# Performance work log

Measured on AMD Instinct MI355X. Metric: run time of the kernel, lower is better.

The kernel has to match this reference:

```python
import jax, jax.numpy as jnp
import numpy as np


def setup_inputs() -> dict:
    key = jax.random.key(0)
    k1, k2 = jax.random.split(key)
    x = jax.random.normal(k1, (8, 2500, 100), dtype=jnp.float32)          # [B, L, E]
    label_feature = jax.random.normal(k2, (8922, 100), dtype=jnp.float32)  # [N, E]
    return {"x": x, "label_feature": label_feature}


def reference(x, label_feature):
    # scores: [B, N, L] = label_feature @ x^T (broadcast query over batch), unscaled
    scores = jnp.einsum("ne,ble->bnl", label_feature, x)
    alpha = jax.nn.softmax(scores, axis=2)  # softmax over sequence length
    # m: [B, N, E] = alpha @ x
    m = jnp.einsum("bnl,ble->bne", alpha, x)
    return m
```

## Files before the change

### kernel.cpp

```cpp
#include <hip/hip_runtime.h>
#include <math.h>
#include <stdint.h>

typedef __attribute__((ext_vector_type(8))) _Float16 half8;
typedef __attribute__((ext_vector_type(4))) _Float16 half4;
typedef __attribute__((ext_vector_type(4))) float f32x4;

constexpr int Bb = 8, Ll = 2500, Ee = 100, Nn = 8922;
constexpr int LP = 2560, EP = 128;
constexpr int NP = 9024;
constexpr int VE = 112;
constexpr int LT = 64;
constexpr int NTILES = LP / LT;
constexpr int NTB = 192;
constexpr int NH = 3;

constexpr size_t SZ_LF = (size_t)NP * EP * 2;
constexpr size_t SZ_XW = (size_t)Bb * LP * EP * 2;
constexpr size_t SZ_XT = (size_t)Bb * VE * LP * 2;
constexpr size_t OFF_XW = SZ_LF;
constexpr size_t OFF_XT = OFF_XW + SZ_XW;
constexpr size_t WS_NEED = OFF_XT + SZ_XT;

__device__ __forceinline__ void gload16(const void* g, void* l) {
    __builtin_amdgcn_global_load_lds(
        (const __attribute__((address_space(1))) uint32_t*)g,
        (__attribute__((address_space(3))) uint32_t*)l, 16, 0, 0);
}

__global__ __launch_bounds__(256)
void prep_all(const float* __restrict__ x, const float* __restrict__ lf,
              uint32_t* __restrict__ dlf, uint32_t* __restrict__ dxw,
              uint16_t* __restrict__ dxt) {
    if (blockIdx.y == Bb) {
        for (int idx = blockIdx.x * 256 + threadIdx.x; idx < NP * 64; idx += 40 * 256) {
            int n = idx >> 6, ep = idx & 63;
            int e0 = 2 * ep, e1 = e0 + 1;
            float f0 = (n < Nn && e0 < Ee) ? lf[(size_t)n * Ee + e0] : 0.f;
            float f1 = (n < Nn && e1 < Ee) ? lf[(size_t)n * Ee + e1] : (e1 == 127 ? 1.0f : 0.f);
            union { _Float16 h[2]; uint32_t u; } cv;
            cv.h[0] = (_Float16)f0; cv.h[1] = (_Float16)f1;
            dlf[idx] = cv.u;
        }
        return;
    }
    __shared__ float lx[64][101];
    const int l0 = blockIdx.x * 64;
    const int b  = blockIdx.y;
    for (int i = threadIdx.x; i < 64 * Ee; i += 256) {
        int ll = i / Ee, e = i - ll * Ee;
        int l = l0 + ll;
        lx[ll][e] = (l < Ll) ? x[((size_t)b * Ll + l) * Ee + e] : 0.f;
    }
    __syncthreads();
    for (int i = threadIdx.x; i < 64 * 64; i += 256) {
        int row = i >> 6, ep = i & 63;
        int l = l0 + row;
        int e0 = 2 * ep, e1 = e0 + 1;
        float f0 = (e0 < Ee) ? lx[row][e0] : 0.f;
        float f1;
        if (e1 < Ee)        f1 = lx[row][e1];
        else if (e1 == 127) f1 = (l < Ll) ? 0.f : -20000.f;
        else                f1 = 0.f;
        union { _Float16 h[2]; uint32_t u; } cv;
        cv.h[0] = (_Float16)f0; cv.h[1] = (_Float16)f1;
        int boff = (4 * ep) ^ ((row & 7) << 4);
        dxw[((size_t)b * LP + l) * 64 + (boff >> 2)] = cv.u;
    }
    for (int i = threadIdx.x; i < VE * 64; i += 256) {
        int e = i >> 6, ll = i & 63;
        float v = (e < Ee) ? lx[ll][e] : 0.f;
        uint32_t boff = (uint32_t)((2 * ll) ^ ((e & 7) << 4));
        union { _Float16 h; uint16_t u; } cv; cv.h = (_Float16)v;
        dxt[((size_t)b * VE + e) * LP + l0 + (boff >> 1)] = cv.u;
    }
}

__global__ __launch_bounds__(256, 2)
void cwa_mfma(const uint16_t* __restrict__ lf16, const uint16_t* __restrict__ xw,
              const uint16_t* __restrict__ xt, float* __restrict__ out) {
    __shared__ __align__(128) char smem[71680];
    const int tid = threadIdx.x, lane = tid & 63, w = tid >> 6;
    const int g = lane >> 4, nl = lane & 15;
    const int b = blockIdx.y;
    const int n_base = blockIdx.x * NTB + w * 48;

    const char* xwb = (const char*)(xw + (size_t)b * LP * EP);
    const char* xtb = (const char*)(xt + (size_t)b * VE * LP);

    auto stage_k = [&](int t, int p) {
        const char* kg = xwb + (size_t)t * (LT * EP * 2);
        char* kbuf = smem + p * 16384;
#pragma unroll
        for (int i = 0; i < 4; i++) {
            int off = i * 4096 + tid * 16;
            gload16(kg + off, kbuf + off);
        }
    };
    auto stage_v = [&](int t) {
        const char* vg = xtb + (size_t)t * (LT * 2);
        char* vbuf = smem + 32768;
#pragma unroll
        for (int i = 0; i < 3; i++) {
            int u = i * 256 + tid;
            gload16(vg + (size_t)(u >> 3) * (LP * 2) + (u & 7) * 16, vbuf + u * 16);
        }
        if (tid < 128) {
            int u = 768 + tid;
            gload16(vg + (size_t)(u >> 3) * (LP * 2) + (u & 7) * 16, vbuf + u * 16);
        }
    };

    stage_k(0, 0);
    stage_v(0);

    half8 qf[NH][4];
#pragma unroll
    for (int nh = 0; nh < NH; nh++) {
        const uint16_t* qr = lf16 + (size_t)(n_base + 16 * nh + nl) * EP + 8 * g;
#pragma unroll
        for (int ks = 0; ks < 4; ks++) qf[nh][ks] = *(const half8*)(qr + 32 * ks);
    }
    asm volatile("s_waitcnt vmcnt(0)" ::: "memory");
    __syncthreads();
    stage_k(1, 1);

    f32x4 oacc[NH][7];
#pragma unroll
    for (int nh = 0; nh < NH; nh++)
#pragma unroll
        for (int es = 0; es < 7; es++) oacc[nh][es] = f32x4{0.f, 0.f, 0.f, 0.f};
    float m_i[NH] = {-INFINITY, -INFINITY, -INFINITY}, s_i[NH] = {0.f, 0.f, 0.f};

    const char* vb = smem + 32768;
    char* pb = smem + 47104 + w * 6144;
    const int swp = (nl & 7) << 4;

    for (int t = 0; t < NTILES; t++) {
        const int p = t & 1;
        const char* kb = smem + p * 16384;

        f32x4 sacc[NH][4];
#pragma unroll
        for (int nh = 0; nh < NH; nh++)
#pragma unroll
            for (int ls = 0; ls < 4; ls++) sacc[nh][ls] = f32x4{0.f, 0.f, 0.f, 0.f};
#pragma unroll
        for (int ls = 0; ls < 4; ls++) {
            const int lrow = 16 * ls + nl;
            const char* kr = kb + lrow * 256;
            const int sw = (lrow & 7) << 4;
#pragma unroll
            for (int ks = 0; ks < 4; ks++) {
                half8 kf = *(const half8*)(kr + ((64 * ks + 16 * g) ^ sw));
                sacc[0][ls] = __builtin_amdgcn_mfma_f32_16x16x32_f16(kf, qf[0][ks], sacc[0][ls], 0, 0, 0);
                sacc[1][ls] = __builtin_amdgcn_mfma_f32_16x16x32_f16(kf, qf[1][ks], sacc[1][ls], 0, 0, 0);
                sacc[2][ls] = __builtin_amdgcn_mfma_f32_16x16x32_f16(kf, qf[2][ks], sacc[2][ls], 0, 0, 0);
            }
        }

        float tm[NH];
#pragma unroll
        for (int nh = 0; nh < NH; nh++) {
            float a0 = fmaxf(fmaxf(sacc[nh][0][0], sacc[nh][0][1]), fmaxf(sacc[nh][0][2], sacc[nh][0][3]));
            float a1 = fmaxf(fmaxf(sacc[nh][1][0], sacc[nh][1][1]), fmaxf(sacc[nh][1][2], sacc[nh][1][3]));
            float a2 = fmaxf(fmaxf(sacc[nh][2][0], sacc[nh][2][1]), fmaxf(sacc[nh][2][2], sacc[nh][2][3]));
            float a3 = fmaxf(fmaxf(sacc[nh][3][0], sacc[nh][3][1]), fmaxf(sacc[nh][3][2], sacc[nh][3][3]));
            float tmv = fmaxf(fmaxf(a0, a1), fmaxf(a2, a3));
            tmv = fmaxf(tmv, __shfl_xor(tmv, 16, 64));
            tmv = fmaxf(tmv, __shfl_xor(tmv, 32, 64));
            tm[nh] = tmv;
        }

        if (!__all((tm[0] <= m_i[0] + 8.f) && (tm[1] <= m_i[1] + 8.f) && (tm[2] <= m_i[2] + 8.f))) {
#pragma unroll
            for (int nh = 0; nh < NH; nh++) {
                const float mn = fmaxf(m_i[nh], tm[nh]);
                const float sc = __expf(m_i[nh] - mn);
                m_i[nh] = mn;
                s_i[nh] *= sc;
#pragma unroll
                for (int r = 0; r < 4; r++) {
                    float scr = __shfl(sc, 4 * g + r, 64);
#pragma unroll
                    for (int es = 0; es < 7; es++) oacc[nh][es][r] *= scr;
                }
            }
        }

#pragma unroll
        for (int nh = 0; nh < NH; nh++) {
            float ts = 0.f;
            half4 ph[4];
#pragma unroll
            for (int ls = 0; ls < 4; ls++)
#pragma unroll
                for (int r = 0; r < 4; r++) {
                    float pv = __expf(sacc[nh][ls][r] - m_i[nh]);
                    ts += pv;
                    ph[ls][r] = (_Float16)pv;
                }
            ts += __shfl_xor(ts, 16, 64);
            ts += __shfl_xor(ts, 32, 64);
            s_i[nh] += ts;
#pragma unroll
            for (int ls = 0; ls < 4; ls++)
                *(half4*)(pb + (16 * nh + nl) * 128 + ((32 * ls + 8 * g) ^ swp)) = ph[ls];
        }

#pragma unroll
        for (int kl = 0; kl < 2; kl++) {
            half8 pf0 = *(const half8*)(pb + nl * 128 + ((64 * kl + 16 * g) ^ swp));
            half8 pf1 = *(const half8*)(pb + (16 + nl) * 128 + ((64 * kl + 16 * g) ^ swp));
            half8 pf2 = *(const half8*)(pb + (32 + nl) * 128 + ((64 * kl + 16 * g) ^ swp));
#pragma unroll
            for (int es = 0; es < 7; es++) {
                const int er = 16 * es + nl;
                half8 vf = *(const half8*)(vb + er * 128 + ((64 * kl + 16 * g) ^ ((er & 7) << 4)));
                oacc[0][es] = __builtin_amdgcn_mfma_f32_16x16x32_f16(pf0, vf, oacc[0][es], 0, 0, 0);
                oacc[1][es] = __builtin_amdgcn_mfma_f32_16x16x32_f16(pf1, vf, oacc[1][es], 0, 0, 0);
                oacc[2][es] = __builtin_amdgcn_mfma_f32_16x16x32_f16(pf2, vf, oacc[2][es], 0, 0, 0);
            }
        }

        __syncthreads();
        const int tv = min(t + 1, NTILES - 1);
        const int tk = min(t + 2, NTILES - 1);
        stage_v(tv);
        stage_k(tk, p);
        asm volatile("s_waitcnt vmcnt(4)" ::: "memory");
        __syncthreads();
    }

#pragma unroll
    for (int nh = 0; nh < NH; nh++) {
        const float inv = 1.0f / s_i[nh];
#pragma unroll
        for (int r = 0; r < 4; r++) {
            const float invr = __shfl(inv, 4 * g + r, 64);
            const int n = n_base + 16 * nh + 4 * g + r;
            if (n < Nn) {
#pragma unroll
                for (int es = 0; es < 7; es++) {
                    const int e = 16 * es + nl;
                    if (e < Ee) out[((size_t)b * Nn + n) * Ee + e] = oacc[nh][es][r] * invr;
                }
            }
        }
    }
}

constexpr int FNT = 16, FLT = 64, FLTP = 65;
__global__ __launch_bounds__(256)
void cwa_fwd(const float* __restrict__ x, const float* __restrict__ lf,
             float* __restrict__ out) {
    __shared__ float q[FNT][Ee];
    __shared__ float xts[Ee][FLTP];
    __shared__ float pl[FNT][FLT];
    const int tid = threadIdx.x, lane = tid & 63, w = tid >> 6;
    const int b = blockIdx.y, n0 = blockIdx.x * FNT;
    for (int idx = tid; idx < FNT * Ee; idx += 256) {
        int nl = idx / Ee, e = idx - nl * Ee;
        int n = n0 + nl;
        q[nl][e] = (n < Nn) ? lf[n * Ee + e] : 0.0f;
    }
    float m_i[4], s_i[4], a0[4], a1[4];
#pragma unroll
    for (int i = 0; i < 4; i++) { m_i[i] = -INFINITY; s_i[i] = 0.f; a0[i] = 0.f; a1[i] = 0.f; }
    const float* xb = x + (size_t)b * Ll * Ee;
    const bool hi_ok = lane < (Ee - 64);
    for (int l0 = 0; l0 < Ll; l0 += FLT) {
        const int nrows = min(FLT, Ll - l0);
        __syncthreads();
        for (int idx = tid; idx < FLT * (Ee / 4); idx += 256) {
            int r = idx / (Ee / 4), c4 = idx - r * (Ee / 4);
            float4 v = make_float4(0.f, 0.f, 0.f, 0.f);
            if (r < nrows) v = *reinterpret_cast<const float4*>(xb + (size_t)(l0 + r) * Ee + c4 * 4);
            xts[c4 * 4 + 0][r] = v.x; xts[c4 * 4 + 1][r] = v.y;
            xts[c4 * 4 + 2][r] = v.z; xts[c4 * 4 + 3][r] = v.w;
        }
        __syncthreads();
        float sc[4] = {0.f, 0.f, 0.f, 0.f};
        for (int e = 0; e < Ee; e++) {
            float xv = xts[e][lane];
#pragma unroll
            for (int i = 0; i < 4; i++) sc[i] = fmaf(q[4 * w + i][e], xv, sc[i]);
        }
        const bool valid = lane < nrows;
#pragma unroll
        for (int i = 0; i < 4; i++) {
            float s = valid ? sc[i] : -INFINITY;
            float tmv = s;
#pragma unroll
            for (int msk = 32; msk >= 1; msk >>= 1) tmv = fmaxf(tmv, __shfl_xor(tmv, msk, 64));
            float mn = fmaxf(m_i[i], tmv);
            float pp = __expf(s - mn);
            float sm = pp;
#pragma unroll
            for (int msk = 32; msk >= 1; msk >>= 1) sm += __shfl_xor(sm, msk, 64);
            float scl = __expf(m_i[i] - mn);
            s_i[i] = s_i[i] * scl + sm; m_i[i] = mn;
            a0[i] *= scl; a1[i] *= scl;
            pl[4 * w + i][lane] = pp;
        }
        __syncthreads();
#pragma unroll 4
        for (int l = 0; l < FLT; l++) {
            float xv0 = xts[lane][l];
            float xv1 = hi_ok ? xts[64 + lane][l] : 0.f;
#pragma unroll
            for (int i = 0; i < 4; i++) {
                float pv = pl[4 * w + i][l];
                a0[i] = fmaf(pv, xv0, a0[i]); a1[i] = fmaf(pv, xv1, a1[i]);
            }
        }
    }
#pragma unroll
    for (int i = 0; i < 4; i++) {
        int n = n0 + 4 * w + i;
        if (n >= Nn) continue;
        float inv = 1.0f / s_i[i];
        size_t base = ((size_t)b * Nn + n) * Ee;
        out[base + lane] = a0[i] * inv;
        if (hi_ok) out[base + 64 + lane] = a1[i] * inv;
    }
}

extern "C" void kernel_launch(void* const* d_in, const int* in_sizes, int n_in,
                              void* d_out, int out_size, void* d_ws, size_t ws_size,
                              hipStream_t stream) {
    const float* x  = (const float*)d_in[0];
    const float* lf = (const float*)d_in[1];
    float* out = (float*)d_out;
    if (ws_size >= WS_NEED) {
        uint32_t* dlf = (uint32_t*)d_ws;
        uint32_t* dxw = (uint32_t*)((char*)d_ws + OFF_XW);
        uint16_t* dxt = (uint16_t*)((char*)d_ws + OFF_XT);
        prep_all<<<dim3(LP / 64, Bb + 1), 256, 0, stream>>>(x, lf, dlf, dxw, dxt);
        cwa_mfma<<<dim3(NP / NTB, Bb), 256, 0, stream>>>(
            (const uint16_t*)dlf, (const uint16_t*)dxw, dxt, out);
    } else {
        dim3 grid((Nn + FNT - 1) / FNT, Bb);
        cwa_fwd<<<grid, dim3(256), 0, stream>>>(x, lf, out);
    }
}
```

Measured before the change: 238.6 us.

## Switch attention kernel to 32x32x16 MFMA with register-resident P fragments

Rewrites the fused attention kernel to use 32x32x16 f16 MFMA tiles, with 32 label rows per wave instead of 48 and 128 per block instead of 192. The softmax probabilities are packed with cvt_pkrtz and swapped between half-waves by shuffle to build the A operand directly, so the per-wave LDS buffer for P and its round trip go away. LDS shrinks from 71680 to 49152 bytes, allowing 3 blocks per CU. Other changes: the K swizzle widens to 16 keys, the grid is flattened with batch as the fastest-varying index, and N padding changes. The trade-off is more registers per lane for the 32x32 accumulators and extra cross-lane shuffles.

Result: no change. 234.7 us (-1.6%).

```diff
diff --git a/kernel.cpp b/kernel.cpp
--- a/kernel.cpp
+++ b/kernel.cpp
@@ -3,17 +3,15 @@
 #include <stdint.h>
 
 typedef __attribute__((ext_vector_type(8))) _Float16 half8;
-typedef __attribute__((ext_vector_type(4))) _Float16 half4;
-typedef __attribute__((ext_vector_type(4))) float f32x4;
+typedef __attribute__((ext_vector_type(16))) float f32x16;
+typedef __attribute__((ext_vector_type(4))) uint32_t uint4v;
 
 constexpr int Bb = 8, Ll = 2500, Ee = 100, Nn = 8922;
-constexpr int LP = 2560, EP = 128;
-constexpr int NP = 9024;
+constexpr int LP = 2560, EP = 128, NP = 8960;
 constexpr int VE = 112;
 constexpr int LT = 64;
 constexpr int NTILES = LP / LT;
-constexpr int NTB = 192;
-constexpr int NH = 3;
+constexpr int NTB = 128;
 
 constexpr size_t SZ_LF = (size_t)NP * EP * 2;
 constexpr size_t SZ_XW = (size_t)Bb * LP * EP * 2;
@@ -64,7 +62,7 @@
         else                f1 = 0.f;
         union { _Float16 h[2]; uint32_t u; } cv;
         cv.h[0] = (_Float16)f0; cv.h[1] = (_Float16)f1;
-        int boff = (4 * ep) ^ ((row & 7) << 4);
+        int boff = (4 * ep) ^ ((row & 15) << 4);
         dxw[((size_t)b * LP + l) * 64 + (boff >> 2)] = cv.u;
     }
     for (int i = threadIdx.x; i < VE * 64; i += 256) {
@@ -76,14 +74,15 @@
     }
 }
 
-__global__ __launch_bounds__(256, 2)
+__global__ __launch_bounds__(256, 3)
 void cwa_mfma(const uint16_t* __restrict__ lf16, const uint16_t* __restrict__ xw,
               const uint16_t* __restrict__ xt, float* __restrict__ out) {
-    __shared__ __align__(128) char smem[71680];
+    __shared__ __align__(128) char smem[49152];
     const int tid = threadIdx.x, lane = tid & 63, w = tid >> 6;
-    const int g = lane >> 4, nl = lane & 15;
-    const int b = blockIdx.y;
-    const int n_base = blockIdx.x * NTB + w * 48;
+    const int r31 = lane & 31, hi = lane >> 5;
+    const int o = blockIdx.x;
+    const int b = o & 7, xb = o >> 3;
+    const int n_base = xb * NTB + w * 32;
 
     const char* xwb = (const char*)(xw + (size_t)b * LP * EP);
     const char* xtb = (const char*)(xt + (size_t)b * VE * LP);
@@ -114,112 +113,97 @@
     stage_k(0, 0);
     stage_v(0);
 
-    half8 qf[NH][4];
-#pragma unroll
-    for (int nh = 0; nh < NH; nh++) {
-        const uint16_t* qr = lf16 + (size_t)(n_base + 16 * nh + nl) * EP + 8 * g;
-#pragma unroll
-        for (int ks = 0; ks < 4; ks++) qf[nh][ks] = *(const half8*)(qr + 32 * ks);
+    half8 qf[8];
+    {
+        const uint16_t* qr = lf16 + (size_t)(n_base + r31) * EP + 8 * hi;
+#pragma unroll
+        for (int ks = 0; ks < 8; ks++) qf[ks] = *(const half8*)(qr + 16 * ks);
     }
     asm volatile("s_waitcnt vmcnt(0)" ::: "memory");
     __syncthreads();
     stage_k(1, 1);
 
-    f32x4 oacc[NH][7];
-#pragma unroll
-    for (int nh = 0; nh < NH; nh++)
-#pragma unroll
-        for (int es = 0; es < 7; es++) oacc[nh][es] = f32x4{0.f, 0.f, 0.f, 0.f};
-    float m_i[NH] = {-INFINITY, -INFINITY, -INFINITY}, s_i[NH] = {0.f, 0.f, 0.f};
+    f32x16 oacc[4];
+#pragma unroll
+    for (int eb = 0; eb < 4; eb++)
+#pragma unroll
+        for (int r = 0; r < 16; r++) oacc[eb][r] = 0.f;
+    float m_i = -INFINITY, s_i = 0.f;
 
     const char* vb = smem + 32768;
-    char* pb = smem + 47104 + w * 6144;
-    const int swp = (nl & 7) << 4;
+    const int kkey = r31 & 15;
+    const int vkey = r31 & 7;
 
     for (int t = 0; t < NTILES; t++) {
         const int p = t & 1;
         const char* kb = smem + p * 16384;
 
-        f32x4 sacc[NH][4];
-#pragma unroll
-        for (int nh = 0; nh < NH; nh++)
-#pragma unroll
-            for (int ls = 0; ls < 4; ls++) sacc[nh][ls] = f32x4{0.f, 0.f, 0.f, 0.f};
-#pragma unroll
-        for (int ls = 0; ls < 4; ls++) {
-            const int lrow = 16 * ls + nl;
-            const char* kr = kb + lrow * 256;
-            const int sw = (lrow & 7) << 4;
-#pragma unroll
-            for (int ks = 0; ks < 4; ks++) {
-                half8 kf = *(const half8*)(kr + ((64 * ks + 16 * g) ^ sw));
-                sacc[0][ls] = __builtin_amdgcn_mfma_f32_16x16x32_f16(kf, qf[0][ks], sacc[0][ls], 0, 0, 0);
-                sacc[1][ls] = __builtin_amdgcn_mfma_f32_16x16x32_f16(kf, qf[1][ks], sacc[1][ls], 0, 0, 0);
-                sacc[2][ls] = __builtin_amdgcn_mfma_f32_16x16x32_f16(kf, qf[2][ks], sacc[2][ls], 0, 0, 0);
-            }
-        }
-
-        float tm[NH];
-#pragma unroll
-        for (int nh = 0; nh < NH; nh++) {
-            float a0 = fmaxf(fmaxf(sacc[nh][0][0], sacc[nh][0][1]), fmaxf(sacc[nh][0][2], sacc[nh][0][3]));
-            float a1 = fmaxf(fmaxf(sacc[nh][1][0], sacc[nh][1][1]), fmaxf(sacc[nh][1][2], sacc[nh][1][3]));
-            float a2 = fmaxf(fmaxf(sacc[nh][2][0], sacc[nh][2][1]), fmaxf(sacc[nh][2][2], sacc[nh][2][3]));
-            float a3 = fmaxf(fmaxf(sacc[nh][3][0], sacc[nh][3][1]), fmaxf(sacc[nh][3][2], sacc[nh][3][3]));
-            float tmv = fmaxf(fmaxf(a0, a1), fmaxf(a2, a3));
-            tmv = fmaxf(tmv, __shfl_xor(tmv, 16, 64));
-            tmv = fmaxf(tmv, __shfl_xor(tmv, 32, 64));
-            tm[nh] = tmv;
-        }
-
-        if (!__all((tm[0] <= m_i[0] + 8.f) && (tm[1] <= m_i[1] + 8.f) && (tm[2] <= m_i[2] + 8.f))) {
-#pragma unroll
-            for (int nh = 0; nh < NH; nh++) {
-                const float mn = fmaxf(m_i[nh], tm[nh]);
-                const float sc = __expf(m_i[nh] - mn);
-                m_i[nh] = mn;
-                s_i[nh] *= sc;
-#pragma unroll
-                for (int r = 0; r < 4; r++) {
-                    float scr = __shfl(sc, 4 * g + r, 64);
-#pragma unroll
-                    for (int es = 0; es < 7; es++) oacc[nh][es][r] *= scr;
-                }
-            }
-        }
-
-#pragma unroll
-        for (int nh = 0; nh < NH; nh++) {
-            float ts = 0.f;
-            half4 ph[4];
-#pragma unroll
-            for (int ls = 0; ls < 4; ls++)
-#pragma unroll
-                for (int r = 0; r < 4; r++) {
-                    float pv = __expf(sacc[nh][ls][r] - m_i[nh]);
-                    ts += pv;
-                    ph[ls][r] = (_Float16)pv;
-                }
-            ts += __shfl_xor(ts, 16, 64);
-            ts += __shfl_xor(ts, 32, 64);
-            s_i[nh] += ts;
-#pragma unroll
-            for (int ls = 0; ls < 4; ls++)
-                *(half4*)(pb + (16 * nh + nl) * 128 + ((32 * ls + 8 * g) ^ swp)) = ph[ls];
-        }
-
-#pragma unroll
-        for (int kl = 0; kl < 2; kl++) {
-            half8 pf0 = *(const half8*)(pb + nl * 128 + ((64 * kl + 16 * g) ^ swp));
-            half8 pf1 = *(const half8*)(pb + (16 + nl) * 128 + ((64 * kl + 16 * g) ^ swp));
-            half8 pf2 = *(const half8*)(pb + (32 + nl) * 128 + ((64 * kl + 16 * g) ^ swp));
-#pragma unroll
-            for (int es = 0; es < 7; es++) {
-                const int er = 16 * es + nl;
-                half8 vf = *(const half8*)(vb + er * 128 + ((64 * kl + 16 * g) ^ ((er & 7) << 4)));
-                oacc[0][es] = __builtin_amdgcn_mfma_f32_16x16x32_f16(pf0, vf, oacc[0][es], 0, 0, 0);
-                oacc[1][es] = __builtin_amdgcn_mfma_f32_16x16x32_f16(pf1, vf, oacc[1][es], 0, 0, 0);
-                oacc[2][es] = __builtin_amdgcn_mfma_f32_16x16x32_f16(pf2, vf, oacc[2][es], 0, 0, 0);
+        f32x16 sacc[2];
+#pragma unroll
+        for (int lb = 0; lb < 2; lb++)
+#pragma unroll
+            for (int r = 0; r < 16; r++) sacc[lb][r] = 0.f;
+#pragma unroll
+        for (int lb = 0; lb < 2; lb++) {
+            const char* kr = kb + (32 * lb + r31) * 256;
+#pragma unroll
+            for (int ks = 0; ks < 8; ks++) {
+                half8 kf = *(const half8*)(kr + (((2 * ks + hi) ^ kkey) << 4));
+                sacc[lb] = __builtin_amdgcn_mfma_f32_32x32x16_f16(kf, qf[ks], sacc[lb], 0, 0, 0);
+            }
+        }
+
+        float tmv = -INFINITY;
+#pragma unroll
+        for (int lb = 0; lb < 2; lb++)
+#pragma unroll
+            for (int r = 0; r < 16; r++) tmv = fmaxf(tmv, sacc[lb][r]);
+        tmv = fmaxf(tmv, __shfl_xor(tmv, 32, 64));
+
+        if (!__all(tmv <= m_i + 8.f)) {
+            const float mn = fmaxf(m_i, tmv);
+            const float sc = __expf(m_i - mn);
+            m_i = mn;
+            s_i *= sc;
+#pragma unroll
+            for (int r = 0; r < 16; r++) {
+                float scr = __shfl(sc, (r & 3) + 8 * (r >> 2) + 4 * hi, 64);
+#pragma unroll
+                for (int eb = 0; eb < 4; eb++) oacc[eb][r] *= scr;
+            }
+        }
+
+        half8 pa[4];
+        float ts = 0.f;
+#pragma unroll
+        for (int lb = 0; lb < 2; lb++) {
+            uint32_t c[8], xch[8];
+#pragma unroll
+            for (int i = 0; i < 8; i++) {
+                float p0 = __expf(sacc[lb][2 * i]     - m_i);
+                float p1 = __expf(sacc[lb][2 * i + 1] - m_i);
+                ts += p0 + p1;
+                c[i] = __builtin_bit_cast(uint32_t, __builtin_amdgcn_cvt_pkrtz(p0, p1));
+            }
+#pragma unroll
+            for (int i = 0; i < 8; i++) xch[i] = __shfl_xor(c[i], 32, 64);
+            uint4v wa = {hi ? xch[2] : c[0], hi ? xch[3] : c[1],
+                         hi ? c[2] : xch[0], hi ? c[3] : xch[1]};
+            uint4v wb2 = {hi ? xch[6] : c[4], hi ? xch[7] : c[5],
+                          hi ? c[6] : xch[4], hi ? c[7] : xch[5]};
+            pa[2 * lb]     = __builtin_bit_cast(half8, wa);
+            pa[2 * lb + 1] = __builtin_bit_cast(half8, wb2);
+        }
+        ts += __shfl_xor(ts, 32, 64);
+        s_i += ts;
+
+#pragma unroll
+        for (int eb = 0; eb < 4; eb++) {
+            const char* vr = vb + (32 * eb + r31) * 128;
+#pragma unroll
+            for (int kk = 0; kk < 4; kk++) {
+                half8 vf = *(const half8*)(vr + (((2 * kk + hi) ^ vkey) << 4));
+                oacc[eb] = __builtin_amdgcn_mfma_f32_32x32x16_f16(pa[kk], vf, oacc[eb], 0, 0, 0);
             }
         }
 
@@ -232,20 +216,18 @@
         __syncthreads();
     }
 
-#pragma unroll
-    for (int nh = 0; nh < NH; nh++) {
-        const float inv = 1.0f / s_i[nh];
-#pragma unroll
-        for (int r = 0; r < 4; r++) {
-            const float invr = __shfl(inv, 4 * g + r, 64);
-            const int n = n_base + 16 * nh + 4 * g + r;
-            if (n < Nn) {
-#pragma unroll
-                for (int es = 0; es < 7; es++) {
-                    const int e = 16 * es + nl;
-                    if (e < Ee) out[((size_t)b * Nn + n) * Ee + e] = oacc[nh][es][r] * invr;
-                }
-            }
+    const float inv = 1.0f / s_i;
+#pragma unroll
+    for (int r = 0; r < 16; r++) {
+        const int nrow = (r & 3) + 8 * (r >> 2) + 4 * hi;
+        const float invr = __shfl(inv, nrow, 64);
+        const int n = n_base + nrow;
+        if (n < Nn) {
+            float* orow = out + ((size_t)b * Nn + n) * Ee;
+            orow[r31]      = oacc[0][r] * invr;
+            orow[32 + r31] = oacc[1][r] * invr;
+            orow[64 + r31] = oacc[2][r] * invr;
+            if (r31 < 4) orow[96 + r31] = oacc[3][r] * invr;
         }
     }
 }
@@ -337,7 +319,7 @@
         uint32_t* dxw = (uint32_t*)((char*)d_ws + OFF_XW);
         uint16_t* dxt = (uint16_t*)((char*)d_ws + OFF_XT);
         prep_all<<<dim3(LP / 64, Bb + 1), 256, 0, stream>>>(x, lf, dlf, dxw, dxt);
-        cwa_mfma<<<dim3(NP / NTB, Bb), 256, 0, stream>>>(
+        cwa_mfma<<<dim3((NP / NTB) * Bb), 256, 0, stream>>>(
             (const uint16_t*)dlf, (const uint16_t*)dxw, dxt, out);
     } else {
         dim3 grid((Nn + FNT - 1) / FNT, Bb);
```
